# Optimization experiments

Hardware: AMD Instinct MI355X
Metric: run time of the kernel (lower is better)

Reference implementation:

```python
import jax, jax.numpy as jnp
import numpy as np

N_NODES = 100000
FEAT = 256
HID = 128
REL = 2
BATCH = 20000
K = 10  # filtersize


def setup_inputs() -> dict:
    key = jax.random.key(0)
    k1, k2, k3, k4, k5 = jax.random.split(key, 5)
    nodes = jax.random.randint(k1, (BATCH,), 0, N_NODES)
    neigh_idx = jax.random.randint(k2, (REL, BATCH, K), 0, N_NODES)
    features = jax.random.normal(k3, (N_NODES, FEAT), dtype=jnp.float32)
    W_stc = jax.random.normal(k4, (REL, FEAT, HID), dtype=jnp.float32) * (1.0 / np.sqrt(FEAT))
    W_det = jax.random.normal(k5, (FEAT + REL * HID, HID), dtype=jnp.float32) * (1.0 / np.sqrt(FEAT + REL * HID))
    return {"nodes": nodes, "neigh_idx": neigh_idx, "features": features,
            "W_stc": W_stc, "W_det": W_det}


def reference(nodes, neigh_idx, features, W_stc, W_det):
    # self features: irregular gather [B, F]
    self_feats = features[nodes]
    # per-relation neighbor gather [R, B, K, F] -> mean over sampled neighbors [R, B, F]
    neigh_mean = features[neigh_idx].mean(axis=2)
    # STC layer projection to hidden per relation: [R, B, H]
    neigh_h = jnp.einsum('rbf,rfh->rbh', neigh_mean, W_stc)
    # concat self feats with each relation's neighbor embedding: [B, F + R*H]
    combined = jnp.concatenate(
        [self_feats, jnp.moveaxis(neigh_h, 0, 1).reshape(neigh_h.shape[1], -1)], axis=1)
    # linear + relu (dropout_flag=False -> no dropout)
    return jax.nn.relu(combined @ W_det)
```

## Files before the change

### kernel.cpp

```cpp
#include <hip/hip_runtime.h>
#include <hip/hip_bf16.h>

#define N_NODES 100000
#define FEAT    256
#define HID     128
#define REL     2
#define BATCH   20000
#define KNEI    10

typedef short  bf16x8 __attribute__((ext_vector_type(8)));
typedef _Float16 half8 __attribute__((ext_vector_type(8)));
typedef float  f32x4  __attribute__((ext_vector_type(4)));

__device__ __forceinline__ unsigned short f2h(float x) {
    union { _Float16 h; unsigned short u; } t; t.h = (_Float16)x; return t.u;
}
__device__ __forceinline__ ushort4 pack4h(float a, float b, float c, float d) {
    ushort4 p; p.x = f2h(a); p.y = f2h(b); p.z = f2h(c); p.w = f2h(d); return p;
}

__device__ __forceinline__ unsigned short f2bf(float x) {
    union { float f; unsigned u; } v; v.f = x;
    unsigned r = v.u + 0x7fffu + ((v.u >> 16) & 1u);
    return (unsigned short)(r >> 16);
}
__device__ __forceinline__ ushort4 pack4(float a, float b, float c, float d) {
    ushort4 p; p.x = f2bf(a); p.y = f2bf(b); p.z = f2bf(c); p.w = f2bf(d); return p;
}

__device__ __forceinline__ size_t bswi(int k, int n, int NT) {
    int kt = k >> 5, j = k & 7, hi = (k >> 3) & 3;
    int lane = hi * 16 + (n & 15), nt = n >> 4;
    return ((size_t)(kt * NT + nt) * 64 + lane) * 8 + j;
}


__global__ __launch_bounds__(256) void prep_Bf16(const float* __restrict__ W_stc,
                                                 const float* __restrict__ W_det,
                                                 unsigned short* __restrict__ Bsw_det,
                                                 unsigned short* __restrict__ Bsw_stc) {
    const int blk = blockIdx.x, tid = threadIdx.x;
    if (blk < 64) {
        #pragma unroll
        for (int i = 0; i < 4; ++i) {
            const int idx = blk * 1024 + i * 256 + tid;
            const int k = idx >> 7, n = idx & 127;
            Bsw_det[bswi(k, n, 8)] = f2h(W_det[idx]);
        }
    } else {
        #pragma unroll
        for (int i = 0; i < 4; ++i) {
            const int idx = (blk - 64) * 1024 + i * 256 + tid;
            const int f = idx >> 8, n = idx & 255;
            const int rel = n >> 7, h = n & 127;
            Bsw_stc[bswi(f, n, 16)] = f2h(W_stc[(size_t)(rel * FEAT + f) * HID + h]);
        }
    }
}

#define APROW 264
__global__ __launch_bounds__(256) void prep_P(const float* __restrict__ features,
                                              const unsigned short* __restrict__ Bsw_stc,
                                              unsigned short* __restrict__ P) {
    __shared__ __align__(16) unsigned short Ap[16 * APROW];
    __shared__ __align__(16) unsigned short Cs[16 * 256];
    const int blk = blockIdx.x, tid = threadIdx.x;
    const int w = tid >> 6, lane = tid & 63;
    const float4* F4 = (const float4*)features;

    #pragma unroll
    for (int s = 0; s < 4; ++s) {
        const int g = s * 256 + tid;
        const int row = g >> 6, c4 = g & 63;
        float4 v = F4[(size_t)(blk * 16 + row) * 64 + c4];
        *(ushort4*)(Ap + row * APROW + c4 * 4) = pack4h(v.x, v.y, v.z, v.w);
    }
    __syncthreads();

    const int quad = lane >> 4, l16 = lane & 15;
    const unsigned short* a_base = Ap + l16 * APROW + quad * 8;
    f32x4 acc[4] = {{0,0,0,0},{0,0,0,0},{0,0,0,0},{0,0,0,0}};
    #pragma unroll
    for (int kt = 0; kt < 8; ++kt) {
        half8 a = *(const half8*)(a_base + kt * 32);
        #pragma unroll
        for (int t = 0; t < 4; ++t) {
            const int nt = w + t * 4;
            half8 b = *(const half8*)(Bsw_stc + ((size_t)(kt * 16 + nt) * 64 + lane) * 8);
            acc[t] = __builtin_amdgcn_mfma_f32_16x16x32_f16(a, b, acc[t], 0, 0, 0);
        }
    }
    #pragma unroll
    for (int t = 0; t < 4; ++t) {
        const int nt = w + t * 4;
        #pragma unroll
        for (int r = 0; r < 4; ++r)
            Cs[(quad * 4 + r) * 256 + nt * 16 + l16] = f2h(acc[t][r]);
    }
    __syncthreads();

    const int seg = tid >> 3, part = tid & 7;
    const int row = seg >> 1, rel = seg & 1;
    const unsigned short* src = Cs + row * 256 + rel * 128 + part * 16;
    unsigned short* dst = P + (size_t)rel * N_NODES * HID
                            + (size_t)(blk * 16 + row) * HID + part * 16;
    *(uint4*)(dst)     = *(const uint4*)(src);
    *(uint4*)(dst + 8) = *(const uint4*)(src + 8);
}

#define AROW2 520
__global__ __launch_bounds__(256, 6) void fused2(const int* __restrict__ nodes,
                                                 const int* __restrict__ neigh_idx,
                                                 const float* __restrict__ features,
                                                 const unsigned short* __restrict__ P,
                                                 const unsigned short* __restrict__ Bsw_det,
                                                 float* __restrict__ out) {
    __shared__ __align__(16) unsigned short As[16 * AROW2];
    __shared__ int idxs[336];

    const int blk = blockIdx.x, tid = threadIdx.x;
    const int w = tid >> 6, lane = tid & 63;
    const int grp = lane >> 4, l16 = lane & 15;
    const float4* F4 = (const float4*)features;
    const float inv = 1.0f / (float)KNEI;

    if (tid < 16)       idxs[tid] = nodes[blk * 16 + tid];
    else if (tid < 176) idxs[tid] = neigh_idx[blk * 160 + (tid - 16)];
    else                idxs[tid] = neigh_idx[BATCH * KNEI + blk * 160 + (tid - 176)];
    const int t2 = tid + 256;
    if (t2 < 336)       idxs[t2] = neigh_idx[BATCH * KNEI + blk * 160 + (t2 - 176)];
    __syncthreads();

    #pragma unroll
    for (int e = 0; e < 4; ++e) {
        const int m = w * 4 + e;
        float4 sf = F4[(size_t)idxs[m] * 64 + lane];
        *(ushort4*)(As + m * AROW2 + lane * 4) = pack4h(sf.x, sf.y, sf.z, sf.w);

        #pragma unroll
        for (int r = 0; r < 2; ++r) {
            const int* ir = &idxs[16 + r * 160 + m * KNEI];
            const unsigned short* Pr = P + (size_t)r * N_NODES * HID;
            float acc[8] = {0.f,0.f,0.f,0.f,0.f,0.f,0.f,0.f};
            #pragma unroll
            for (int L = 0; L < 3; ++L) {
                const int kk = L * 4 + grp;
                const int nd = ir[kk < KNEI ? kk : KNEI - 1];
                uint4 raw = *(const uint4*)(Pr + (size_t)nd * HID + l16 * 8);
                float v[8];
                union { unsigned u; _Float16 h[2]; } t;
                t.u = raw.x; v[0] = (float)t.h[0]; v[1] = (float)t.h[1];
                t.u = raw.y; v[2] = (float)t.h[0]; v[3] = (float)t.h[1];
                t.u = raw.z; v[4] = (float)t.h[0]; v[5] = (float)t.h[1];
                t.u = raw.w; v[6] = (float)t.h[0]; v[7] = (float)t.h[1];
                if (L < 2 || lane < 32) {
                    #pragma unroll
                    for (int j = 0; j < 8; ++j) acc[j] += v[j];
                }
            }
            #pragma unroll
            for (int j = 0; j < 8; ++j) acc[j] += __shfl_xor(acc[j], 16);
            #pragma unroll
            for (int j = 0; j < 8; ++j) acc[j] += __shfl_xor(acc[j], 32);
            if (lane < 16) {
                unsigned short* d = As + m * AROW2 + 256 + r * 128 + lane * 8;
                *(ushort4*)(d)     = pack4h(acc[0]*inv, acc[1]*inv, acc[2]*inv, acc[3]*inv);
                *(ushort4*)(d + 4) = pack4h(acc[4]*inv, acc[5]*inv, acc[6]*inv, acc[7]*inv);
            }
        }
    }
    __syncthreads();

    const unsigned short* a_base = As + l16 * AROW2 + grp * 8;
    f32x4 acc0 = (f32x4){0.f,0.f,0.f,0.f};
    f32x4 acc1 = (f32x4){0.f,0.f,0.f,0.f};
    const int nt0 = w, nt1 = w + 4;
    #pragma unroll
    for (int kt = 0; kt < 16; ++kt) {
        half8 a = *(const half8*)(a_base + kt * 32);
        const unsigned short* bk = Bsw_det + ((size_t)(kt * 8) * 64 + lane) * 8;
        half8 b0 = *(const half8*)(bk + (size_t)nt0 * 512);
        half8 b1 = *(const half8*)(bk + (size_t)nt1 * 512);
        acc0 = __builtin_amdgcn_mfma_f32_16x16x32_f16(a, b0, acc0, 0, 0, 0);
        acc1 = __builtin_amdgcn_mfma_f32_16x16x32_f16(a, b1, acc1, 0, 0, 0);
    }
    float* orow = out + (size_t)(blk * 16) * HID;
    #pragma unroll
    for (int r = 0; r < 4; ++r) {
        const int row = grp * 4 + r;
        float v0 = acc0[r], v1 = acc1[r];
        orow[(size_t)row * HID + nt0 * 16 + l16] = v0 > 0.f ? v0 : 0.f;
        orow[(size_t)row * HID + nt1 * 16 + l16] = v1 > 0.f ? v1 : 0.f;
    }
}

#define APAD    8
#define AROW    (768 + APAD)

__device__ __forceinline__ size_t bsw_index(int k, int n) {
    int kt = k >> 5, j = k & 7, hi = (k >> 3) & 3;
    int lane = hi * 16 + (n & 15), nt = n >> 4;
    return ((size_t)(kt * 8 + nt) * 64 + lane) * 8 + j;
}

__global__ __launch_bounds__(256) void prep_B_old(const float* __restrict__ W_stc,
                                                  const float* __restrict__ W_det,
                                                  unsigned short* __restrict__ Bsw) {
    const int blk = blockIdx.x;
    const int tid = threadIdx.x;
    if (blk < 256) {
        const int rel = blk >> 7;
        const int f   = (blk & 127) * 2 + (tid >> 7);
        const int n   = tid & 127;
        const float* ws = W_stc + (size_t)(rel * FEAT + f) * HID;
        const float* wd = W_det + (size_t)(256 + rel * HID) * HID + n;
        float acc = 0.f;
        #pragma unroll
        for (int j = 0; j < HID; ++j) acc += ws[j] * wd[(size_t)j * HID];
        Bsw[bsw_index(256 + rel * 256 + f, n)] = f2bf(acc);
    } else {
        const int base = (blk - 256) * 2048;
        #pragma unroll
        for (int i = 0; i < 8; ++i) {
            const int idx = base + i * 256 + tid;
            const int k = idx >> 7, n = idx & 127;
            Bsw[bsw_index(k, n)] = f2bf(W_det[idx]);
        }
    }
}

__global__ __launch_bounds__(256, 4) void fused_old(const int* __restrict__ nodes,
                                                    const int* __restrict__ neigh_idx,
                                                    const float* __restrict__ features,
                                                    const unsigned short* __restrict__ Bsw,
                                                    float* __restrict__ out) {
    __shared__ unsigned short As[16 * AROW];
    __shared__ int idxs[336];

    const int blk  = blockIdx.x;
    const int tid  = threadIdx.x;
    const int w    = tid >> 6;
    const int lane = tid & 63;
    const float inv = 1.0f / (float)KNEI;

    if (tid < 16)       idxs[tid] = nodes[blk * 16 + tid];
    else if (tid < 176) idxs[tid] = neigh_idx[blk * 160 + (tid - 16)];
    else                idxs[tid] = neigh_idx[BATCH * KNEI + blk * 160 + (tid - 176)];
    const int t2 = tid + 256;
    if (t2 < 336)       idxs[t2] = neigh_idx[BATCH * KNEI + blk * 160 + (t2 - 176)];
    __syncthreads();

    const unsigned lnoff = (unsigned)lane << 4;
    #pragma unroll
    for (int e = 0; e < 4; ++e) {
        const int m = w * 4 + e;
        int ia[11], ib[10];
        ia[0] = idxs[m];
        #pragma unroll
        for (int k = 0; k < KNEI; ++k) ia[1 + k] = idxs[16 + m * KNEI + k];
        #pragma unroll
        for (int k = 0; k < KNEI; ++k) ib[k]     = idxs[176 + m * KNEI + k];

        f32x4 ta[11];
        #pragma unroll
        for (int k = 0; k < 11; ++k) {
            const unsigned voff = ((unsigned)ia[k] << 10) + lnoff;
            asm volatile("global_load_dwordx4 %0, %1, %2"
                         : "=v"(ta[k]) : "v"(voff), "s"(features));
        }
        f32x4 tb[10];
        #pragma unroll
        for (int k = 0; k < KNEI; ++k) {
            const unsigned voff = ((unsigned)ib[k] << 10) + lnoff;
            asm volatile("global_load_dwordx4 %0, %1, %2"
                         : "=v"(tb[k]) : "v"(voff), "s"(features));
        }

        asm volatile("s_waitcnt vmcnt(10)" ::: "memory");
        __builtin_amdgcn_sched_barrier(0);

        f32x4 s0 = ta[1];
        #pragma unroll
        for (int k = 2; k < 11; ++k) s0 += ta[k];

        ushort4* row = (ushort4*)(As + m * AROW);
        row[lane]      = pack4(ta[0][0], ta[0][1], ta[0][2], ta[0][3]);
        row[64 + lane] = pack4(s0[0] * inv, s0[1] * inv, s0[2] * inv, s0[3] * inv);

        asm volatile("s_waitcnt vmcnt(0)" ::: "memory");
        __builtin_amdgcn_sched_barrier(0);

        f32x4 s1 = tb[0];
        #pragma unroll
        for (int k = 1; k < KNEI; ++k) s1 += tb[k];
        row[128 + lane] = pack4(s1[0] * inv, s1[1] * inv, s1[2] * inv, s1[3] * inv);
    }
    __syncthreads();

    const int quad = lane >> 4;
    const int l16  = lane & 15;
    const unsigned short* a_base = As + l16 * AROW + quad * 8;

    f32x4 acc0 = (f32x4){0.f, 0.f, 0.f, 0.f};
    f32x4 acc1 = (f32x4){0.f, 0.f, 0.f, 0.f};
    const int nt0 = w, nt1 = w + 4;

    #pragma unroll
    for (int kt = 0; kt < 24; ++kt) {
        bf16x8 a = *(const bf16x8*)(a_base + kt * 32);
        const unsigned short* bk = Bsw + ((size_t)(kt * 8) * 64 + lane) * 8;
        bf16x8 b0 = *(const bf16x8*)(bk + (size_t)nt0 * 64 * 8);
        bf16x8 b1 = *(const bf16x8*)(bk + (size_t)nt1 * 64 * 8);
        acc0 = __builtin_amdgcn_mfma_f32_16x16x32_bf16(a, b0, acc0, 0, 0, 0);
        acc1 = __builtin_amdgcn_mfma_f32_16x16x32_bf16(a, b1, acc1, 0, 0, 0);
    }

    float* orow = out + (size_t)(blk * 16) * HID;
    #pragma unroll
    for (int r = 0; r < 4; ++r) {
        const int row = quad * 4 + r;
        float v0 = acc0[r];
        float v1 = acc1[r];
        orow[(size_t)row * HID + nt0 * 16 + l16] = v0 > 0.f ? v0 : 0.f;
        orow[(size_t)row * HID + nt1 * 16 + l16] = v1 > 0.f ? v1 : 0.f;
    }
}

extern "C" void kernel_launch(void* const* d_in, const int* in_sizes, int n_in,
                              void* d_out, int out_size, void* d_ws, size_t ws_size,
                              hipStream_t stream) {
    const int*   nodes     = (const int*)d_in[0];
    const int*   neigh_idx = (const int*)d_in[1];
    const float* features  = (const float*)d_in[2];
    const float* W_stc     = (const float*)d_in[3];
    const float* W_det     = (const float*)d_in[4];
    float* out = (float*)d_out;

    const size_t P_BYTES   = (size_t)REL * N_NODES * HID * 2;
    const size_t BD_BYTES  = 512 * 128 * 2;
    const size_t BS_BYTES  = 256 * 256 * 2;
    const size_t WS_NEEDED = P_BYTES + BD_BYTES + BS_BYTES;

    if (ws_size >= WS_NEEDED) {
        unsigned short* P       = (unsigned short*)d_ws;
        unsigned short* Bsw_det = (unsigned short*)((char*)d_ws + P_BYTES);
        unsigned short* Bsw_stc = (unsigned short*)((char*)d_ws + P_BYTES + BD_BYTES);
        prep_Bf16<<<128, 256, 0, stream>>>(W_stc, W_det, Bsw_det, Bsw_stc);
        prep_P<<<N_NODES / 16, 256, 0, stream>>>(features, Bsw_stc, P);
        fused2<<<BATCH / 16, 256, 0, stream>>>(nodes, neigh_idx, features, P, Bsw_det, out);
    } else {
        unsigned short* Bsw = (unsigned short*)d_ws;
        prep_B_old<<<272, 256, 0, stream>>>(W_stc, W_det, Bsw);
        fused_old<<<BATCH / 16, 256, 0, stream>>>(nodes, neigh_idx, features, Bsw, out);
    }
}
```

Measured before the change: 210.5 us.

## Rewrite node projection as persistent per-relation kernel with W_stc staged in LDS

Replaces the per-16-node projection kernel with a persistent grid of 512 blocks. Each block handles one relation, loads that relation's swizzled W_stc slice (64 KB) into shared memory once, then loops over node tiles. The MFMA is transposed so features feed directly from global memory as the B operand, with no LDS staging. Each lane then writes P rows straight to memory with no shared-memory transpose. The goal is to drop repeated global weight reads and LDS round-trips, at the cost of reading each features row twice (once per relation) and running at lower occupancy.

```diff
diff --git a/kernel.cpp b/kernel.cpp
--- a/kernel.cpp
+++ b/kernel.cpp
@@ -38,7 +38,7 @@
 __global__ __launch_bounds__(256) void prep_Bf16(const float* __restrict__ W_stc,
                                                  const float* __restrict__ W_det,
                                                  unsigned short* __restrict__ Bsw_det,
-                                                 unsigned short* __restrict__ Bsw_stc) {
+                                                 unsigned short* __restrict__ Aswz) {
     const int blk = blockIdx.x, tid = threadIdx.x;
     if (blk < 64) {
         #pragma unroll
@@ -48,64 +48,72 @@
             Bsw_det[bswi(k, n, 8)] = f2h(W_det[idx]);
         }
     } else {
-        #pragma unroll
-        for (int i = 0; i < 4; ++i) {
-            const int idx = (blk - 64) * 1024 + i * 256 + tid;
-            const int f = idx >> 8, n = idx & 255;
-            const int rel = n >> 7, h = n & 127;
-            Bsw_stc[bswi(f, n, 16)] = f2h(W_stc[(size_t)(rel * FEAT + f) * HID + h]);
-        }
-    }
-}
-
-#define APROW 264
-__global__ __launch_bounds__(256) void prep_P(const float* __restrict__ features,
-                                              const unsigned short* __restrict__ Bsw_stc,
-                                              unsigned short* __restrict__ P) {
-    __shared__ __align__(16) unsigned short Ap[16 * APROW];
-    __shared__ __align__(16) unsigned short Cs[16 * 256];
-    const int blk = blockIdx.x, tid = threadIdx.x;
-    const int w = tid >> 6, lane = tid & 63;
-    const float4* F4 = (const float4*)features;
-
-    #pragma unroll
-    for (int s = 0; s < 4; ++s) {
-        const int g = s * 256 + tid;
-        const int row = g >> 6, c4 = g & 63;
-        float4 v = F4[(size_t)(blk * 16 + row) * 64 + c4];
-        *(ushort4*)(Ap + row * APROW + c4 * 4) = pack4h(v.x, v.y, v.z, v.w);
-    }
-    __syncthreads();
-
-    const int quad = lane >> 4, l16 = lane & 15;
-    const unsigned short* a_base = Ap + l16 * APROW + quad * 8;
-    f32x4 acc[4] = {{0,0,0,0},{0,0,0,0},{0,0,0,0},{0,0,0,0}};
-    #pragma unroll
-    for (int kt = 0; kt < 8; ++kt) {
-        half8 a = *(const half8*)(a_base + kt * 32);
-        #pragma unroll
-        for (int t = 0; t < 4; ++t) {
-            const int nt = w + t * 4;
-            half8 b = *(const half8*)(Bsw_stc + ((size_t)(kt * 16 + nt) * 64 + lane) * 8);
-            acc[t] = __builtin_amdgcn_mfma_f32_16x16x32_f16(a, b, acc[t], 0, 0, 0);
-        }
-    }
-    #pragma unroll
-    for (int t = 0; t < 4; ++t) {
-        const int nt = w + t * 4;
-        #pragma unroll
-        for (int r = 0; r < 4; ++r)
-            Cs[(quad * 4 + r) * 256 + nt * 16 + l16] = f2h(acc[t][r]);
-    }
-    __syncthreads();
-
-    const int seg = tid >> 3, part = tid & 7;
-    const int row = seg >> 1, rel = seg & 1;
-    const unsigned short* src = Cs + row * 256 + rel * 128 + part * 16;
-    unsigned short* dst = P + (size_t)rel * N_NODES * HID
-                            + (size_t)(blk * 16 + row) * HID + part * 16;
-    *(uint4*)(dst)     = *(const uint4*)(src);
-    *(uint4*)(dst + 8) = *(const uint4*)(src + 8);
+        const int gid = (blk - 64) * 256 + tid;
+        const int rel = gid >> 12;
+        const int kt  = (gid >> 9) & 7;
+        const int mt  = (gid >> 6) & 7;
+        const int lane = gid & 63;
+        const int q = lane >> 4, l16 = lane & 15;
+        unsigned short* dst = Aswz + (size_t)rel * 32768 + ((size_t)(kt * 8 + mt) * 64 + lane) * 8;
+        #pragma unroll
+        for (int j = 0; j < 8; ++j) {
+            dst[j] = f2h(W_stc[(size_t)(rel * FEAT + kt * 32 + q * 8 + j) * HID + mt * 16 + l16]);
+        }
+    }
+}
+
+__global__ __launch_bounds__(256, 2) void prep_P2(const float* __restrict__ features,
+                                                  const unsigned short* __restrict__ Aswz,
+                                                  unsigned short* __restrict__ P) {
+    __shared__ __align__(16) unsigned short Asw[32768];
+    const int b = blockIdx.x;
+    const int rel = b >> 8, chunk = b & 255;
+    const int tid = threadIdx.x, w = tid >> 6, lane = tid & 63;
+    const int q = lane >> 4, l16 = lane & 15;
+
+    {
+        const uint4* src = (const uint4*)(Aswz + (size_t)rel * 32768);
+        uint4* dst = (uint4*)Asw;
+        #pragma unroll
+        for (int i = 0; i < 16; ++i) dst[i * 256 + tid] = src[i * 256 + tid];
+    }
+    __syncthreads();
+
+    unsigned short* Pr = P + (size_t)rel * N_NODES * HID;
+
+    for (int t = chunk * 4 + w; t < 6250; t += 1024) {
+        const int node = t * 16 + l16;
+        const float* frow = features + (size_t)node * FEAT + q * 8;
+
+        half8 bfrag[8];
+        #pragma unroll
+        for (int kt = 0; kt < 8; ++kt) {
+            float4 lo = *(const float4*)(frow + kt * 32);
+            float4 hi = *(const float4*)(frow + kt * 32 + 4);
+            half8 h;
+            h[0] = (_Float16)lo.x; h[1] = (_Float16)lo.y;
+            h[2] = (_Float16)lo.z; h[3] = (_Float16)lo.w;
+            h[4] = (_Float16)hi.x; h[5] = (_Float16)hi.y;
+            h[6] = (_Float16)hi.z; h[7] = (_Float16)hi.w;
+            bfrag[kt] = h;
+        }
+
+        f32x4 acc[8] = {{0,0,0,0},{0,0,0,0},{0,0,0,0},{0,0,0,0},
+                        {0,0,0,0},{0,0,0,0},{0,0,0,0},{0,0,0,0}};
+        #pragma unroll
+        for (int kt = 0; kt < 8; ++kt) {
+            #pragma unroll
+            for (int mt = 0; mt < 8; ++mt) {
+                half8 a = *(const half8*)(Asw + ((size_t)(kt * 8 + mt) * 64 + lane) * 8);
+                acc[mt] = __builtin_amdgcn_mfma_f32_16x16x32_f16(a, bfrag[kt], acc[mt], 0, 0, 0);
+            }
+        }
+
+        unsigned short* prow = Pr + (size_t)node * HID + q * 4;
+        #pragma unroll
+        for (int mt = 0; mt < 8; ++mt)
+            *(ushort4*)(prow + mt * 16) = pack4h(acc[mt][0], acc[mt][1], acc[mt][2], acc[mt][3]);
+    }
 }
 
 #define AROW2 520
@@ -338,15 +346,15 @@
 
     const size_t P_BYTES   = (size_t)REL * N_NODES * HID * 2;
     const size_t BD_BYTES  = 512 * 128 * 2;
-    const size_t BS_BYTES  = 256 * 256 * 2;
-    const size_t WS_NEEDED = P_BYTES + BD_BYTES + BS_BYTES;
+    const size_t AS_BYTES  = (size_t)REL * 32768 * 2;
+    const size_t WS_NEEDED = P_BYTES + BD_BYTES + AS_BYTES;
 
     if (ws_size >= WS_NEEDED) {
         unsigned short* P       = (unsigned short*)d_ws;
         unsigned short* Bsw_det = (unsigned short*)((char*)d_ws + P_BYTES);
-        unsigned short* Bsw_stc = (unsigned short*)((char*)d_ws + P_BYTES + BD_BYTES);
-        prep_Bf16<<<128, 256, 0, stream>>>(W_stc, W_det, Bsw_det, Bsw_stc);
-        prep_P<<<N_NODES / 16, 256, 0, stream>>>(features, Bsw_stc, P);
+        unsigned short* Aswz    = (unsigned short*)((char*)d_ws + P_BYTES + BD_BYTES);
+        prep_Bf16<<<96, 256, 0, stream>>>(W_stc, W_det, Bsw_det, Aswz);
+        prep_P2<<<512, 256, 0, stream>>>(features, Aswz, P);
         fused2<<<BATCH / 16, 256, 0, stream>>>(nodes, neigh_idx, features, P, Bsw_det, out);
     } else {
         unsigned short* Bsw = (unsigned short*)d_ws;
```

Result: slower. 249.1 us (+18.3%).

## Process 64 nodes per block in prep_P to reuse weight fragments across tiles

Applied to the files above, without the earlier changes.

The precompute kernel that projects all node features through W_stc now handles 64 rows per block instead of 16. Each wave loads its four B fragments once per k-step and applies them to four row tiles, which cuts repeated global reads of the weights. The output goes through a per-wave padded shared staging buffer one tile at a time. The cost is more accumulator registers (64 floats) and more LDS per block, which can lower occupancy, plus bounds handling for a tail block.

```diff
diff --git a/kernel.cpp b/kernel.cpp
--- a/kernel.cpp
+++ b/kernel.cpp
@@ -59,53 +59,79 @@
 }
 
 #define APROW 264
-__global__ __launch_bounds__(256) void prep_P(const float* __restrict__ features,
-                                              const unsigned short* __restrict__ Bsw_stc,
-                                              unsigned short* __restrict__ P) {
-    __shared__ __align__(16) unsigned short Ap[16 * APROW];
-    __shared__ __align__(16) unsigned short Cs[16 * 256];
+#define CSROW 68
+__global__ __launch_bounds__(256, 4) void prep_P3(const float* __restrict__ features,
+                                                  const unsigned short* __restrict__ Bsw_stc,
+                                                  unsigned short* __restrict__ P) {
+    __shared__ __align__(16) unsigned short Ap[64 * APROW];
+    __shared__ __align__(16) unsigned short Cs[4][16 * CSROW];
+
     const int blk = blockIdx.x, tid = threadIdx.x;
     const int w = tid >> 6, lane = tid & 63;
+    const int q = lane >> 4, l16 = lane & 15;
+    const int base = blk * 64;
+    const int nloc = (N_NODES - base) < 64 ? (N_NODES - base) : 64;
+    const int ntile = nloc >> 4;
     const float4* F4 = (const float4*)features;
 
     #pragma unroll
-    for (int s = 0; s < 4; ++s) {
-        const int g = s * 256 + tid;
+    for (int i = 0; i < 16; ++i) {
+        const int g = i * 256 + tid;
         const int row = g >> 6, c4 = g & 63;
-        float4 v = F4[(size_t)(blk * 16 + row) * 64 + c4];
-        *(ushort4*)(Ap + row * APROW + c4 * 4) = pack4h(v.x, v.y, v.z, v.w);
-    }
-    __syncthreads();
-
-    const int quad = lane >> 4, l16 = lane & 15;
-    const unsigned short* a_base = Ap + l16 * APROW + quad * 8;
-    f32x4 acc[4] = {{0,0,0,0},{0,0,0,0},{0,0,0,0},{0,0,0,0}};
+        if (row < nloc) {
+            float4 v = F4[(size_t)(base + row) * 64 + c4];
+            *(ushort4*)(Ap + row * APROW + c4 * 4) = pack4h(v.x, v.y, v.z, v.w);
+        }
+    }
+    __syncthreads();
+
+    f32x4 acc[4][4];
+    #pragma unroll
+    for (int t = 0; t < 4; ++t)
+        #pragma unroll
+        for (int j = 0; j < 4; ++j) acc[t][j] = (f32x4){0.f, 0.f, 0.f, 0.f};
+
     #pragma unroll
     for (int kt = 0; kt < 8; ++kt) {
-        half8 a = *(const half8*)(a_base + kt * 32);
-        #pragma unroll
-        for (int t = 0; t < 4; ++t) {
-            const int nt = w + t * 4;
-            half8 b = *(const half8*)(Bsw_stc + ((size_t)(kt * 16 + nt) * 64 + lane) * 8);
-            acc[t] = __builtin_amdgcn_mfma_f32_16x16x32_f16(a, b, acc[t], 0, 0, 0);
-        }
-    }
-    #pragma unroll
-    for (int t = 0; t < 4; ++t) {
-        const int nt = w + t * 4;
-        #pragma unroll
-        for (int r = 0; r < 4; ++r)
-            Cs[(quad * 4 + r) * 256 + nt * 16 + l16] = f2h(acc[t][r]);
-    }
-    __syncthreads();
-
-    const int seg = tid >> 3, part = tid & 7;
-    const int row = seg >> 1, rel = seg & 1;
-    const unsigned short* src = Cs + row * 256 + rel * 128 + part * 16;
-    unsigned short* dst = P + (size_t)rel * N_NODES * HID
-                            + (size_t)(blk * 16 + row) * HID + part * 16;
-    *(uint4*)(dst)     = *(const uint4*)(src);
-    *(uint4*)(dst + 8) = *(const uint4*)(src + 8);
+        half8 bb[4];
+        #pragma unroll
+        for (int t4 = 0; t4 < 4; ++t4) {
+            const int nt = w * 4 + t4;
+            bb[t4] = *(const half8*)(Bsw_stc + ((size_t)(kt * 16 + nt) * 64 + lane) * 8);
+        }
+        #pragma unroll
+        for (int tile = 0; tile < 4; ++tile) {
+            half8 a = *(const half8*)(Ap + (tile * 16 + l16) * APROW + kt * 32 + q * 8);
+            #pragma unroll
+            for (int t4 = 0; t4 < 4; ++t4)
+                acc[tile][t4] = __builtin_amdgcn_mfma_f32_16x16x32_f16(a, bb[t4], acc[tile][t4], 0, 0, 0);
+        }
+    }
+
+    const int rel_w = w >> 1;
+    const int colbase = (w & 1) * 64;
+    unsigned short* Pw = P + (size_t)rel_w * N_NODES * HID;
+    unsigned short* Cw = Cs[w];
+    const int nl = lane >> 2, seg = lane & 3;
+
+    #pragma unroll
+    for (int tile = 0; tile < 4; ++tile) {
+        #pragma unroll
+        for (int t4 = 0; t4 < 4; ++t4)
+            #pragma unroll
+            for (int r = 0; r < 4; ++r)
+                Cw[(q * 4 + r) * CSROW + t4 * 16 + l16] = f2h(acc[tile][t4][r]);
+        asm volatile("s_waitcnt lgkmcnt(0)" ::: "memory");
+        __builtin_amdgcn_sched_barrier(0);
+
+        if (tile < ntile) {
+            const int gnode = base + tile * 16 + nl;
+            const unsigned short* src = Cw + nl * CSROW + seg * 16;
+            unsigned short* dst = Pw + (size_t)gnode * HID + colbase + seg * 16;
+            *(uint4*)(dst)     = *(const uint4*)(src);
+            *(uint4*)(dst + 8) = *(const uint4*)(src + 8);
+        }
+    }
 }
 
 #define AROW2 520
@@ -346,7 +372,7 @@
         unsigned short* Bsw_det = (unsigned short*)((char*)d_ws + P_BYTES);
         unsigned short* Bsw_stc = (unsigned short*)((char*)d_ws + P_BYTES + BD_BYTES);
         prep_Bf16<<<128, 256, 0, stream>>>(W_stc, W_det, Bsw_det, Bsw_stc);
-        prep_P<<<N_NODES / 16, 256, 0, stream>>>(features, Bsw_stc, P);
+        prep_P3<<<(N_NODES + 63) / 64, 256, 0, stream>>>(features, Bsw_stc, P);
         fused2<<<BATCH / 16, 256, 0, stream>>>(nodes, neigh_idx, features, P, Bsw_det, out);
     } else {
         unsigned short* Bsw = (unsigned short*)d_ws;
```

Measured after the change: 216.5 us. 1.03x slower.
